# Kernel tuning notes

Measured on AMD Instinct MI355X. Metric: run time of the kernel, lower is better.

## Reference

```python
import jax, jax.numpy as jnp
import numpy as np

N_SRC = 100000
N_DST = 100000
E = 1600000
D_IN = 128
D_REL = 128
K = 8        # num_heads
D_OUT = 16   # out_dim per head; K*D_OUT = 128
SLOPE = 0.2  # LeakyReLU negative slope


def setup_inputs() -> dict:
    key = jax.random.key(0)
    ks = jax.random.split(key, 11)
    s = 0.05  # weight init scale
    return {
        "feat_src": jax.random.normal(ks[0], (N_SRC, D_IN), jnp.float32),
        "feat_dst": jax.random.normal(ks[1], (N_DST, D_IN), jnp.float32),
        "feat_rel": jax.random.normal(ks[2], (D_REL,), jnp.float32),
        "W_src": jax.random.normal(ks[3], (D_IN, K * D_OUT), jnp.float32) * s,
        "b_src": jnp.zeros((K * D_OUT,), jnp.float32),
        "W_dst": jax.random.normal(ks[4], (D_IN, K * D_OUT), jnp.float32) * s,
        "b_dst": jnp.zeros((K * D_OUT,), jnp.float32),
        "W_rel": jax.random.normal(ks[5], (D_REL, 2 * K * D_OUT), jnp.float32) * s,
        "b_rel": jnp.zeros((2 * K * D_OUT,), jnp.float32),
        "src_idx": jax.random.randint(ks[6], (E,), 0, N_SRC, dtype=jnp.int32),
        "dst_idx": jax.random.randint(ks[7], (E,), 0, N_DST, dtype=jnp.int32),
    }


def reference(feat_src, feat_dst, feat_rel, W_src, b_src, W_dst, b_dst,
              W_rel, b_rel, src_idx, dst_idx):
    # Linear projections (feat_drop = 0 -> identity)
    fs = (feat_src @ W_src + b_src).reshape(-1, K, D_OUT)   # (N_src, K, D)
    fd = (feat_dst @ W_dst + b_dst).reshape(-1, K, D_OUT)   # (N_dst, K, D)
    attn = (feat_rel @ W_rel + b_rel).reshape(K, 2 * D_OUT)  # (K, 2D)

    el = jnp.einsum('nkd,kd->nk', fs, attn[:, :D_OUT])  # (N_src, K)
    er = jnp.einsum('nkd,kd->nk', fd, attn[:, D_OUT:])  # (N_dst, K)

    # Per-edge scores: u_add_v then LeakyReLU
    e = el[src_idx] + er[dst_idx]                        # (E, K)
    e = jnp.where(e >= 0, e, SLOPE * e)

    # edge_softmax: softmax over incoming edges per destination node
    emax = jax.ops.segment_max(e, dst_idx, num_segments=N_DST)  # (N_dst, K)
    a = jnp.exp(e - emax[dst_idx])                               # (E, K)
    asum = jax.ops.segment_sum(a, dst_idx, num_segments=N_DST)   # (N_dst, K)
    a = a / asum[dst_idx]

    # u_mul_e + sum aggregation
    msg = fs[src_idx] * a[:, :, None]                            # (E, K, D)
    out = jax.ops.segment_sum(msg, dst_idx, num_segments=N_DST)  # (N_dst, K, D)
    return out.reshape(N_DST, K * D_OUT)
```

## Files before the change

### kernel.cpp

```cpp
#include <hip/hip_runtime.h>
#include <hip/hip_fp16.h>
#include <hip/hip_bf16.h>

#define SLOPE 0.2f
#define EPB 16384
#define LDA 136
#define CAPLG 12

typedef short bf16x8 __attribute__((ext_vector_type(8)));
typedef float f32x4 __attribute__((ext_vector_type(4)));

__device__ __forceinline__ unsigned short f2bf(float x) {
    unsigned u = __float_as_uint(x);
    u += 0x7FFFu + ((u >> 16) & 1u);
    return (unsigned short)(u >> 16);
}

__global__ void prep_kernel(const float* __restrict__ feat_rel,
                            const float* __restrict__ W_rel,
                            const float* __restrict__ b_rel,
                            float* __restrict__ attn,
                            const float* __restrict__ W_src,
                            unsigned short* __restrict__ WtS,
                            const float* __restrict__ W_dst,
                            unsigned short* __restrict__ WtD,
                            int* __restrict__ bcur) {
    int bx = blockIdx.x;
    if (bx < 128) {
        const float* W = (bx < 64) ? W_src : W_dst;
        unsigned short* Wt = (bx < 64) ? WtS : WtD;
        int t = (bx & 63) * 256 + threadIdx.x;
        int n = t >> 7, k = t & 127;
        Wt[n * 128 + k] = f2bf(W[k * 128 + n]);
    } else if (bx == 128) {
        int j = threadIdx.x;
        float acc = b_rel[j];
        for (int d = 0; d < 128; ++d)
            acc = fmaf(feat_rel[d], W_rel[d * 256 + j], acc);
        attn[j] = acc;
    } else {
#pragma unroll
        for (int i = 0; i < 4; ++i) {
            int j = threadIdx.x + i * 256;
            bcur[j] = j << CAPLG;
        }
    }
}

__global__ __launch_bounds__(256) void gemm_mfma_kernel(
    const float* __restrict__ featS, const unsigned short* __restrict__ WtS,
    const float* __restrict__ bS,
    const float* __restrict__ featD, const unsigned short* __restrict__ WtD,
    const float* __restrict__ bD,
    const float* __restrict__ attn, __half* __restrict__ fs,
    float* __restrict__ el, float* __restrict__ er,
    int Ms, int Md, int nbs)
{
    __shared__ unsigned short sA[64 * LDA];
    __shared__ unsigned short sB[128 * LDA];
    __shared__ float sAtt[128];

    int bx = blockIdx.x;
    const float* feat; const unsigned short* Wt; const float* bias;
    __half* f_out; float* e_out; int attn_off, M, row0;
    if (bx < nbs) {
        feat = featS; Wt = WtS; bias = bS; f_out = fs; e_out = el;
        attn_off = 0; M = Ms; row0 = bx * 64;
    } else {
        feat = featD; Wt = WtD; bias = bD; f_out = nullptr; e_out = er;
        attn_off = 16; M = Md; row0 = (bx - nbs) * 64;
    }

    int t = threadIdx.x;

    if (t < 128) sAtt[t] = attn[(t >> 4) * 32 + attn_off + (t & 15)];

#pragma unroll
    for (int i = 0; i < 8; ++i) {
        int idx = t + i * 256;
        int row = idx >> 5, k4 = idx & 31;
        int grow = row0 + row;
        float4 v = {0.f, 0.f, 0.f, 0.f};
        if (grow < M) v = *(const float4*)(feat + (size_t)grow * 128 + k4 * 4);
        ushort4 b;
        b.x = f2bf(v.x); b.y = f2bf(v.y); b.z = f2bf(v.z); b.w = f2bf(v.w);
        *(ushort4*)&sA[row * LDA + k4 * 4] = b;
    }
#pragma unroll
    for (int i = 0; i < 8; ++i) {
        int idx = t + i * 256;
        int n = idx >> 4, koff = (idx & 15) * 8;
        *(uint4*)&sB[n * LDA + koff] = *(const uint4*)&Wt[n * 128 + koff];
    }
    __syncthreads();

    int wv = t >> 6, lane = t & 63;
    int m = lane & 15, quad = lane >> 4;
    int n0 = wv * 32;

    f32x4 acc[2][4];
#pragma unroll
    for (int ct = 0; ct < 2; ++ct)
#pragma unroll
        for (int rt = 0; rt < 4; ++rt) acc[ct][rt] = (f32x4){0.f, 0.f, 0.f, 0.f};

#pragma unroll
    for (int ks = 0; ks < 4; ++ks) {
        bf16x8 a[4], b[2];
#pragma unroll
        for (int rt = 0; rt < 4; ++rt)
            a[rt] = *(const bf16x8*)&sA[(rt * 16 + m) * LDA + ks * 32 + quad * 8];
#pragma unroll
        for (int ct = 0; ct < 2; ++ct)
            b[ct] = *(const bf16x8*)&sB[(n0 + ct * 16 + m) * LDA + ks * 32 + quad * 8];
#pragma unroll
        for (int ct = 0; ct < 2; ++ct)
#pragma unroll
            for (int rt = 0; rt < 4; ++rt)
                acc[ct][rt] = __builtin_amdgcn_mfma_f32_16x16x32_bf16(
                    a[rt], b[ct], acc[ct][rt], 0, 0, 0);
    }

    __syncthreads();
    __half* sF = (__half*)sA;
#pragma unroll
    for (int ct = 0; ct < 2; ++ct) {
        int col = n0 + ct * 16 + m;
        float bias_v = bias[col];
#pragma unroll
        for (int rt = 0; rt < 4; ++rt) {
            f32x4 c = acc[ct][rt];
#pragma unroll
            for (int r = 0; r < 4; ++r)
                sF[(rt * 16 + quad * 4 + r) * LDA + col] = __float2half(c[r] + bias_v);
        }
    }
    __syncthreads();

    int mrem = M - row0;

    if (f_out) {
#pragma unroll
        for (int i = 0; i < 4; ++i) {
            int idx = t + i * 256;
            int row = idx >> 4, c8 = (idx & 15) * 8;
            if (row < mrem) {
                uint4 v = *(const uint4*)&sF[row * LDA + c8];
                *(uint4*)(f_out + (size_t)(row0 + row) * 128 + c8) = v;
            }
        }
    }
#pragma unroll
    for (int i = 0; i < 2; ++i) {
        int p = t + i * 256;
        int row = p >> 3, h = p & 7;
        if (row < mrem) {
            const __half* fp = &sF[row * LDA + h * 16];
            const float* ap = &sAtt[h * 16];
            float acc2 = 0.f;
#pragma unroll
            for (int j = 0; j < 16; ++j)
                acc2 = fmaf((float)fp[j], ap[j], acc2);
            e_out[(size_t)(row0 + row) * 8 + h] = acc2;
        }
    }
}

__global__ __launch_bounds__(1024) void part_kernel(
    const int* __restrict__ src_idx, const int* __restrict__ dst_idx,
    int* __restrict__ bcur, int* __restrict__ part, int ne)
{
    __shared__ int hist[1024];
    __shared__ int base[1024];
    int tid = threadIdx.x;
    hist[tid] = 0;
    int e0 = blockIdx.x * EPB;
    int myS[16], myD[16];
    __syncthreads();
#pragma unroll
    for (int i = 0; i < 16; ++i) {
        int e = e0 + i * 1024 + tid;
        if (e < ne) {
            myS[i] = src_idx[e];
            myD[i] = dst_idx[e];
            atomicAdd(&hist[myD[i] >> 7], 1);
        } else myD[i] = -1;
    }
    __syncthreads();
    {
        int c = hist[tid];
        if (c > 0) {
            base[tid] = atomicAdd(&bcur[tid], c);
            hist[tid] = 0;
        }
    }
    __syncthreads();
#pragma unroll
    for (int i = 0; i < 16; ++i) {
        if (myD[i] >= 0) {
            int b = myD[i] >> 7;
            int slot = base[b] + atomicAdd(&hist[b], 1);
            part[slot] = myS[i] | ((myD[i] & 127) << 20);
        }
    }
}

__global__ __launch_bounds__(256) void place_kernel(
    const int* __restrict__ part, const int* __restrict__ bcur,
    int* __restrict__ csr, int* __restrict__ roff, int* __restrict__ deg,
    int n_dst)
{
    int b = blockIdx.x;
    int node0 = b << 7;
    int tid = threadIdx.x;
    __shared__ int cnt[128];
    __shared__ int off[128];
    if (tid < 128) cnt[tid] = 0;
    int pstart = b << CAPLG;
    int pend = bcur[b];
    __syncthreads();

    for (int pi = pstart + tid; pi < pend; pi += 256)
        atomicAdd(&cnt[part[pi] >> 20], 1);
    __syncthreads();

    if (tid < 128) off[tid] = cnt[tid];
    __syncthreads();
    for (int o = 1; o < 128; o <<= 1) {
        int x = 0;
        if (tid < 128 && tid >= o) x = off[tid - o];
        __syncthreads();
        if (tid < 128) off[tid] += x;
        __syncthreads();
    }
    if (tid < 128) {
        int excl = off[tid] - cnt[tid];
        off[tid] = excl;
        int node = node0 + tid;
        if (node < n_dst) {
            roff[node] = pstart + excl;
            deg[node]  = cnt[tid];
        }
        cnt[tid] = 0;
    }
    __syncthreads();

    for (int pi = pstart + tid; pi < pend; pi += 256) {
        int val = part[pi];
        int dl = val >> 20;
        int fine = atomicAdd(&cnt[dl], 1);
        csr[pstart + off[dl] + fine] = val & 0xFFFFF;
    }
}

__global__ __launch_bounds__(256) void agg_kernel(
    const __half* __restrict__ fs, const float* __restrict__ el,
    const float* __restrict__ er, const int* __restrict__ roff,
    const int* __restrict__ deg, const int* __restrict__ csr,
    float* __restrict__ out, int n)
{
    int lane = threadIdx.x & 63;
    int wv = threadIdx.x >> 6;
    int g = lane >> 4;
    int q = lane & 15;
    int h = q >> 1;
    int node = blockIdx.x * 16 + wv * 4 + g;
    bool alive = node < n;
    int start = 0, d = 0;
    float er8 = 0.f;
    if (alive) {
        start = roff[node];
        d = deg[node];
        er8 = er[(size_t)node * 8 + h];
    }

    float acc[8] = {0.f, 0.f, 0.f, 0.f, 0.f, 0.f, 0.f, 0.f};
    float wsum = 0.f;
    int i = 0;
    for (; i + 4 <= d; i += 4) {
        int s[4]; float ex[4]; uint4 v[4];
#pragma unroll
        for (int j = 0; j < 4; ++j)
            s[j] = __builtin_nontemporal_load(csr + start + i + j);
#pragma unroll
        for (int j = 0; j < 4; ++j)
            ex[j] = el[(size_t)s[j] * 8 + h];
#pragma unroll
        for (int j = 0; j < 4; ++j)
            v[j] = *(const uint4*)(fs + (size_t)s[j] * 128 + q * 8);
#pragma unroll
        for (int j = 0; j < 4; ++j) {
            float x = ex[j] + er8;
            x = (x < 0.f) ? SLOPE * x : x;
            float w = __expf(x);
            const __half* hp = (const __half*)&v[j];
#pragma unroll
            for (int k = 0; k < 8; ++k)
                acc[k] = fmaf(w, (float)hp[k], acc[k]);
            wsum += w;
        }
    }
    for (; i < d; ++i) {
        int s0 = __builtin_nontemporal_load(csr + start + i);
        float x = el[(size_t)s0 * 8 + h] + er8;
        x = (x < 0.f) ? SLOPE * x : x;
        float w0 = __expf(x);
        uint4 v0 = *(const uint4*)(fs + (size_t)s0 * 128 + q * 8);
        const __half* hp = (const __half*)&v0;
#pragma unroll
        for (int k = 0; k < 8; ++k)
            acc[k] = fmaf(w0, (float)hp[k], acc[k]);
        wsum += w0;
    }
    if (alive) {
        float inv = (d > 0) ? 1.0f / wsum : 0.f;
        f32x4 o0 = {acc[0] * inv, acc[1] * inv, acc[2] * inv, acc[3] * inv};
        f32x4 o1 = {acc[4] * inv, acc[5] * inv, acc[6] * inv, acc[7] * inv};
        __builtin_nontemporal_store(o0, (f32x4*)(out + (size_t)node * 128 + q * 8));
        __builtin_nontemporal_store(o1, (f32x4*)(out + (size_t)node * 128 + q * 8 + 4));
    }
}

extern "C" void kernel_launch(void* const* d_in, const int* in_sizes, int n_in,
                              void* d_out, int out_size, void* d_ws, size_t ws_size,
                              hipStream_t stream) {
    const float* feat_src = (const float*)d_in[0];
    const float* feat_dst = (const float*)d_in[1];
    const float* feat_rel = (const float*)d_in[2];
    const float* W_src    = (const float*)d_in[3];
    const float* b_src    = (const float*)d_in[4];
    const float* W_dst    = (const float*)d_in[5];
    const float* b_dst    = (const float*)d_in[6];
    const float* W_rel    = (const float*)d_in[7];
    const float* b_rel    = (const float*)d_in[8];
    const int*   src_idx  = (const int*)d_in[9];
    const int*   dst_idx  = (const int*)d_in[10];
    float* out = (float*)d_out;

    int n_src = in_sizes[0] / 128;
    int n_dst = in_sizes[1] / 128;
    int ne    = in_sizes[9];
    int nbuck = (n_dst + 127) >> 7;
    size_t slab = (size_t)nbuck << CAPLG;

    char* w = (char*)d_ws;
    auto alloc = [&](size_t b) { char* p = w; w += (b + 255) & ~(size_t)255; return p; };
    __half* fs   = (__half*)alloc((size_t)n_src * 128 * 2);
    float*  el   = (float*)alloc((size_t)n_src * 8 * 4);
    float*  er   = (float*)alloc((size_t)n_dst * 8 * 4);
    float*  attn = (float*)alloc(256 * 4);
    unsigned short* WtS = (unsigned short*)alloc(128 * 128 * 2);
    unsigned short* WtD = (unsigned short*)alloc(128 * 128 * 2);
    int*    deg  = (int*)alloc((size_t)n_dst * 4);
    int*    roff = (int*)alloc((size_t)n_dst * 4);
    int*    bcur = (int*)alloc(1024 * 4);
    int*    csr  = (int*)alloc(slab * 4);
    int*    part = (int*)alloc(slab * 4);

    prep_kernel<<<130, 256, 0, stream>>>(
        feat_rel, W_rel, b_rel, attn, W_src, WtS, W_dst, WtD, bcur);

    int nbs = (n_src + 63) / 64, nbd = (n_dst + 63) / 64;
    gemm_mfma_kernel<<<nbs + nbd, 256, 0, stream>>>(
        feat_src, WtS, b_src, feat_dst, WtD, b_dst, attn,
        fs, el, er, n_src, n_dst, nbs);

    part_kernel<<<(ne + EPB - 1) / EPB, 1024, 0, stream>>>(src_idx, dst_idx, bcur, part, ne);
    place_kernel<<<nbuck, 256, 0, stream>>>(part, bcur, csr, roff, deg, n_dst);

    agg_kernel<<<(n_dst + 15) / 16, 256, 0, stream>>>(
        fs, el, er, roff, deg, csr, out, n_dst);
}
```

Baseline: 298.7 us.

## Fuse edge partitioning into GEMM kernel as extra blocks to overlap work

Merges the edge-bucketing partition step into the projection GEMM launch by appending extra blocks that do the histogram and scatter, with edges-per-block cut from 16384 to 4096 to match 256 threads. Shared memory becomes one raw buffer reused by both roles. The aim is to drop a kernel launch and let the memory-bound partition run alongside the MFMA GEMM blocks. In exchange, partition blocks now need four times as many global atomics on the bucket counters and share the GEMM's larger shared-memory footprint, which may limit occupancy.

```diff
diff --git a/kernel.cpp b/kernel.cpp
--- a/kernel.cpp
+++ b/kernel.cpp
@@ -3,7 +3,7 @@
 #include <hip/hip_bf16.h>
 
 #define SLOPE 0.2f
-#define EPB 16384
+#define EPB 4096
 #define LDA 136
 #define CAPLG 12
 
@@ -47,20 +47,64 @@
     }
 }
 
-__global__ __launch_bounds__(256) void gemm_mfma_kernel(
+#define SMEM_BYTES ((64 * LDA + 128 * LDA) * 2 + 128 * 4)
+
+__global__ __launch_bounds__(256) void gemm_part_kernel(
     const float* __restrict__ featS, const unsigned short* __restrict__ WtS,
     const float* __restrict__ bS,
     const float* __restrict__ featD, const unsigned short* __restrict__ WtD,
     const float* __restrict__ bD,
     const float* __restrict__ attn, __half* __restrict__ fs,
     float* __restrict__ el, float* __restrict__ er,
-    int Ms, int Md, int nbs)
+    int Ms, int Md, int nbs, int ngemm,
+    const int* __restrict__ src_idx, const int* __restrict__ dst_idx,
+    int* __restrict__ bcur, int* __restrict__ part, int ne)
 {
-    __shared__ unsigned short sA[64 * LDA];
-    __shared__ unsigned short sB[128 * LDA];
-    __shared__ float sAtt[128];
+    __shared__ __align__(16) unsigned char smem[SMEM_BYTES];
 
     int bx = blockIdx.x;
+    int t = threadIdx.x;
+
+    if (bx >= ngemm) {
+        int* hist = (int*)smem;
+        int* base = hist + 1024;
+        for (int i = t; i < 1024; i += 256) hist[i] = 0;
+        int e0 = (bx - ngemm) * EPB;
+        int myS[16], myD[16];
+        __syncthreads();
+#pragma unroll
+        for (int i = 0; i < 16; ++i) {
+            int e = e0 + i * 256 + t;
+            if (e < ne) {
+                myS[i] = src_idx[e];
+                myD[i] = dst_idx[e];
+                atomicAdd(&hist[myD[i] >> 7], 1);
+            } else myD[i] = -1;
+        }
+        __syncthreads();
+        for (int b = t; b < 1024; b += 256) {
+            int c = hist[b];
+            if (c > 0) {
+                base[b] = atomicAdd(&bcur[b], c);
+                hist[b] = 0;
+            }
+        }
+        __syncthreads();
+#pragma unroll
+        for (int i = 0; i < 16; ++i) {
+            if (myD[i] >= 0) {
+                int b = myD[i] >> 7;
+                int slot = base[b] + atomicAdd(&hist[b], 1);
+                part[slot] = myS[i] | ((myD[i] & 127) << 20);
+            }
+        }
+        return;
+    }
+
+    unsigned short* sA = (unsigned short*)smem;
+    unsigned short* sB = sA + 64 * LDA;
+    float* sAtt = (float*)(smem + (64 * LDA + 128 * LDA) * 2);
+
     const float* feat; const unsigned short* Wt; const float* bias;
     __half* f_out; float* e_out; int attn_off, M, row0;
     if (bx < nbs) {
@@ -70,8 +114,6 @@
         feat = featD; Wt = WtD; bias = bD; f_out = nullptr; e_out = er;
         attn_off = 16; M = Md; row0 = (bx - nbs) * 64;
     }
-
-    int t = threadIdx.x;
 
     if (t < 128) sAtt[t] = attn[(t >> 4) * 32 + attn_off + (t & 15)];
 
@@ -162,45 +204,6 @@
             for (int j = 0; j < 16; ++j)
                 acc2 = fmaf((float)fp[j], ap[j], acc2);
             e_out[(size_t)(row0 + row) * 8 + h] = acc2;
-        }
-    }
-}
-
-__global__ __launch_bounds__(1024) void part_kernel(
-    const int* __restrict__ src_idx, const int* __restrict__ dst_idx,
-    int* __restrict__ bcur, int* __restrict__ part, int ne)
-{
-    __shared__ int hist[1024];
-    __shared__ int base[1024];
-    int tid = threadIdx.x;
-    hist[tid] = 0;
-    int e0 = blockIdx.x * EPB;
-    int myS[16], myD[16];
-    __syncthreads();
-#pragma unroll
-    for (int i = 0; i < 16; ++i) {
-        int e = e0 + i * 1024 + tid;
-        if (e < ne) {
-            myS[i] = src_idx[e];
-            myD[i] = dst_idx[e];
-            atomicAdd(&hist[myD[i] >> 7], 1);
-        } else myD[i] = -1;
-    }
-    __syncthreads();
-    {
-        int c = hist[tid];
-        if (c > 0) {
-            base[tid] = atomicAdd(&bcur[tid], c);
-            hist[tid] = 0;
-        }
-    }
-    __syncthreads();
-#pragma unroll
-    for (int i = 0; i < 16; ++i) {
-        if (myD[i] >= 0) {
-            int b = myD[i] >> 7;
-            int slot = base[b] + atomicAdd(&hist[b], 1);
-            part[slot] = myS[i] | ((myD[i] & 127) << 20);
         }
     }
 }
@@ -361,11 +364,13 @@
         feat_rel, W_rel, b_rel, attn, W_src, WtS, W_dst, WtD, bcur);
 
     int nbs = (n_src + 63) / 64, nbd = (n_dst + 63) / 64;
-    gemm_mfma_kernel<<<nbs + nbd, 256, 0, stream>>>(
+    int ngemm = nbs + nbd;
+    int nparts = (ne + EPB - 1) / EPB;
+    gemm_part_kernel<<<ngemm + nparts, 256, 0, stream>>>(
         feat_src, WtS, b_src, feat_dst, WtD, b_dst, attn,
-        fs, el, er, n_src, n_dst, nbs);
-
-    part_kernel<<<(ne + EPB - 1) / EPB, 1024, 0, stream>>>(src_idx, dst_idx, bcur, part, ne);
+        fs, el, er, n_src, n_dst, nbs, ngemm,
+        src_idx, dst_idx, bcur, part, ne);
+
     place_kernel<<<nbuck, 256, 0, stream>>>(part, bcur, csr, roff, deg, n_dst);
 
     agg_kernel<<<(n_dst + 15) / 16, 256, 0, stream>>>(
```

After: 292.9 us. Within noise of the previous version (-1.9%).
